# Performance work log

Hardware: AMD Instinct MI355X
Metric: run time of the kernel (lower is better)

Reference implementation:

```python
import jax, jax.numpy as jnp
import numpy as np

N = 50000
E = 1600000
IN_DIM = 32
EDGE_DIM = 32
HID = 64
OUT = 32


def setup_inputs() -> dict:
    key = jax.random.key(0)
    ks = jax.random.split(key, 12)
    x = jax.random.normal(ks[0], (N, IN_DIM), dtype=jnp.float32)
    edge_index = jax.random.randint(ks[1], (2, E), 0, N, dtype=jnp.int64)
    edge_attr = jax.random.normal(ks[2], (E, EDGE_DIM), dtype=jnp.float32)
    # MLP params: Linear(64->64), Linear(64->128), Linear(128->64), Linear(64->32)
    def lin(k, fan_in, fan_out):
        lim = 1.0 / np.sqrt(fan_in)
        kw, kb = jax.random.split(k)
        W = jax.random.uniform(kw, (fan_in, fan_out), minval=-lim, maxval=lim, dtype=jnp.float32)
        b = jax.random.uniform(kb, (fan_out,), minval=-lim, maxval=lim, dtype=jnp.float32)
        return W, b
    W1, b1 = lin(ks[3], IN_DIM + EDGE_DIM, HID)
    W2, b2 = lin(ks[4], HID, 2 * HID)
    W3, b3 = lin(ks[5], 2 * HID, HID)
    W4, b4 = lin(ks[6], HID, OUT)
    return {"x": x, "edge_index": edge_index, "edge_attr": edge_attr,
            "W1": W1, "b1": b1, "W2": W2, "b2": b2,
            "W3": W3, "b3": b3, "W4": W4, "b4": b4}


def reference(x, edge_index, edge_attr, W1, b1, W2, b2, W3, b3, W4, b4):
    # PyG MessagePassing (source_to_target): x_i = x[edge_index[1]] (target),
    # messages aggregated (mean) at target nodes edge_index[1].
    dst = edge_index[1]
    x_i = x[dst]                                   # [E, IN_DIM] gather
    m = jnp.concatenate([x_i, edge_attr], axis=-1)  # [E, 64]
    # 4-layer MLP with ReLU (dropout = identity at inference)
    m = jax.nn.relu(m @ W1 + b1)                   # [E, 64]
    m = jax.nn.relu(m @ W2 + b2)                   # [E, 128]
    m = jax.nn.relu(m @ W3 + b3)                   # [E, 64]
    m = jax.nn.relu(m @ W4 + b4)                   # [E, 32]
    # mean scatter to target nodes
    sums = jax.ops.segment_sum(m, dst, num_segments=N)          # [N, 32]
    cnt = jax.ops.segment_sum(jnp.ones((E,), m.dtype), dst, num_segments=N)
    out = sums / jnp.maximum(cnt, 1.0)[:, None]
    return out
```

## Files before the change

### kernel.cpp

```cpp
#include <hip/hip_runtime.h>
#include <hip/hip_bf16.h>

typedef __attribute__((ext_vector_type(8))) unsigned short u16x8;
typedef __attribute__((ext_vector_type(8))) __bf16 bf16x8;
typedef __attribute__((ext_vector_type(4))) float f32x4;

__device__ __forceinline__ unsigned pack_bf2(float lo, float hi) {
  unsigned a = __float_as_uint(lo) + 0x8000u;
  unsigned b = __float_as_uint(hi) + 0x8000u;
  return __builtin_amdgcn_perm(b, a, 0x07060302);
}

__device__ __forceinline__ unsigned short f2bf(float f) {
  unsigned u = __float_as_uint(f);
  return (unsigned short)((u + 0x7fffu + ((u >> 16) & 1u)) >> 16);
}

__device__ __forceinline__ int aswz(int row, int feat, int stride) {
  return row * stride + (((feat >> 3) ^ (row & 7)) << 4) + (feat & 7) * 2;
}

__global__ __launch_bounds__(256)
void prep_hist(const float* __restrict__ W1, const float* __restrict__ W2,
               const float* __restrict__ W3, const float* __restrict__ W4,
               unsigned short* __restrict__ wt,
               const int* __restrict__ ei, int* __restrict__ histI, int E, int N) {
  const int tid = threadIdx.x;
  const int i = blockIdx.x * 256 + tid;
  if (i < 22528) {
    float v; int n, k, K, base;
    if (i < 4096)       { n = i >> 6, k = i & 63;  K = 64;  base = 0;     v = W1[k * 64 + n]; }
    else if (i < 12288) { int j = i - 4096;  n = j >> 6, k = j & 63;  K = 64;  base = 4096;  v = W2[k * 128 + n]; }
    else if (i < 20480) { int j = i - 12288; n = j >> 7, k = j & 127; K = 128; base = 12288; v = W3[k * 64 + n]; }
    else                { int j = i - 20480; n = j >> 6, k = j & 63;  K = 64;  base = 20480; v = W4[k * 32 + n]; }
    int o = base + n * K + ((((k >> 3) ^ (n & 7)) << 3) + (k & 7));
    wt[o] = f2bf(v);
  }
  const int xcd = blockIdx.x & 7, kblk = blockIdx.x >> 3;
  const int nchunks = gridDim.x >> 3;
  const int chunk = (((E + nchunks - 1) / nchunks) + 3) & ~3;
  const int eBeg = kblk * chunk;
  const int eEnd = min(eBeg + chunk, E);
  const int dLo = (int)((long)xcd * N / 8);
  const int dHi = (int)((long)(xcd + 1) * N / 8);
  int e0 = eBeg + tid * 4;
  for (; e0 + 3 < eEnd; e0 += 1024) {
    const int4 d4 = *(const int4*)(ei + E + e0);
    if (d4.x >= dLo && d4.x < dHi) atomicAdd(&histI[d4.x], 1);
    if (d4.y >= dLo && d4.y < dHi) atomicAdd(&histI[d4.y], 1);
    if (d4.z >= dLo && d4.z < dHi) atomicAdd(&histI[d4.z], 1);
    if (d4.w >= dLo && d4.w < dHi) atomicAdd(&histI[d4.w], 1);
  }
  for (int e = e0; e < eEnd; ++e) {
    const int d = ei[E + e];
    if (d >= dLo && d < dHi) atomicAdd(&histI[d], 1);
  }
}

__global__ void scan_blocks(const int* __restrict__ histI, int* __restrict__ row_start,
                            int* __restrict__ blockSums, int N) {
  __shared__ int wsum[4];
  const int lane = threadIdx.x & 63, w = threadIdx.x >> 6;
  const int i0 = blockIdx.x * 2048 + threadIdx.x * 8;
  int v[8];
#pragma unroll
  for (int j = 0; j < 8; ++j) { int i = i0 + j; v[j] = (i < N) ? histI[i] : 0; }
  int s = 0;
#pragma unroll
  for (int j = 0; j < 8; ++j) { int t = v[j]; v[j] = s; s += t; }
  int ss = s;
#pragma unroll
  for (int d = 1; d < 64; d <<= 1) { int t = __shfl_up(ss, d, 64); if (lane >= d) ss += t; }
  if (lane == 63) wsum[w] = ss;
  __syncthreads();
  int wOff = 0;
#pragma unroll
  for (int k = 0; k < 4; ++k) if (k < w) wOff += wsum[k];
  const int tOff = wOff + (ss - s);
#pragma unroll
  for (int j = 0; j < 8; ++j) { int i = i0 + j; if (i < N) row_start[i] = tOff + v[j]; }
  if (threadIdx.x == 255) blockSums[blockIdx.x] = wOff + ss;
}

__global__ __launch_bounds__(256)
void fill_kernel(const int* __restrict__ ei, int* __restrict__ row_start,
                 const int* __restrict__ blockSums, int2* __restrict__ edlist,
                 float* __restrict__ out, int E, int N, int nb) {
  __shared__ int spre[32];
  if (threadIdx.x == 0) {
    int acc = 0;
    for (int k = 0; k < nb; ++k) { spre[k] = acc; acc += blockSums[k]; }
  }
  __syncthreads();
  const int tid = threadIdx.x;
  const int Ntot4 = N * 8;
  for (int i = blockIdx.x * 256 + tid; i < Ntot4; i += gridDim.x * 256)
    ((float4*)out)[i] = make_float4(0.f, 0.f, 0.f, 0.f);

  const int xcd = blockIdx.x & 7, kblk = blockIdx.x >> 3;
  const int nchunks = gridDim.x >> 3;
  const int chunk = (((E + nchunks - 1) / nchunks) + 3) & ~3;
  const int eBeg = kblk * chunk;
  const int eEnd = min(eBeg + chunk, E);
  const int dLo = (int)((long)xcd * N / 8);
  const int dHi = (int)((long)(xcd + 1) * N / 8);
  int e0 = eBeg + tid * 4;
  for (; e0 + 3 < eEnd; e0 += 1024) {
    const int4 d4 = *(const int4*)(ei + E + e0);
    const int dv[4] = {d4.x, d4.y, d4.z, d4.w};
#pragma unroll
    for (int j = 0; j < 4; ++j) {
      const int d = dv[j];
      if (d >= dLo && d < dHi) {
        const int pos = atomicAdd(&row_start[d], 1) + spre[d >> 11];
        edlist[pos] = make_int2(e0 + j, d);
      }
    }
  }
  for (int e = e0; e < eEnd; ++e) {
    const int d = ei[E + e];
    if (d >= dLo && d < dHi) {
      const int pos = atomicAdd(&row_start[d], 1) + spre[d >> 11];
      edlist[pos] = make_int2(e, d);
    }
  }
}

template <int MT, int KS, int SS, int DS>
__device__ __forceinline__ void mlp_layer(const unsigned char* src, unsigned char* dst,
                                          const unsigned char* wl, const float* biasL, int lane) {
  const int edge = lane & 15, g = lane >> 4;
  asm volatile("s_waitcnt lgkmcnt(0)" ::: "memory");
  u16x8 bfrag[KS];
#pragma unroll
  for (int ks = 0; ks < KS; ++ks)
    bfrag[ks] = *(const u16x8*)(src + aswz(edge, ks * 32 + g * 8, SS));
#pragma unroll
  for (int mt = 0; mt < MT; ++mt) {
    const int n = mt * 16 + edge;
    u16x8 af[KS];
#pragma unroll
    for (int ks = 0; ks < KS; ++ks)
      af[ks] = *(const u16x8*)(wl + n * (KS * 64) + (((ks * 4 + g) ^ (edge & 7)) << 4));
    const float4 bv = *(const float4*)(biasL + mt * 16 + g * 4);
    f32x4 acc = {bv.x, bv.y, bv.z, bv.w};
    __builtin_amdgcn_s_setprio(1);
#pragma unroll
    for (int ks = 0; ks < KS; ++ks)
      acc = __builtin_amdgcn_mfma_f32_16x16x32_bf16(
          __builtin_bit_cast(bf16x8, af[ks]), __builtin_bit_cast(bf16x8, bfrag[ks]),
          acc, 0, 0, 0);
    __builtin_amdgcn_s_setprio(0);
    const int fb = mt * 16 + g * 4;
    uint2 q;
    q.x = pack_bf2(fmaxf(acc[0], 0.f), fmaxf(acc[1], 0.f));
    q.y = pack_bf2(fmaxf(acc[2], 0.f), fmaxf(acc[3], 0.f));
    *(uint2*)(dst + aswz(edge, fb, DS)) = q;
  }
}

__device__ __forceinline__ void load_tile(int ebase, int E, const int2* __restrict__ edlist,
                                          const float* __restrict__ x, const float* __restrict__ ea,
                                          const int* __restrict__ histI,
                                          int lane, float4& xa, float4& xb, float4& ya, float4& yb,
                                          int& dstA, int& cntA) {
  const int el = ebase + (lane >> 2);
  const int part = lane & 3;
  xa = make_float4(0.f, 0.f, 0.f, 0.f); xb = xa; ya = xa; yb = xa;
  if (el < E) {
    const int2 ed = edlist[el];
    const float4* xp = (const float4*)(x + (size_t)ed.y * 32 + part * 8);
    xa = xp[0]; xb = xp[1];
    const float4* ep = (const float4*)(ea + (size_t)ed.x * 32 + part * 8);
    ya = ep[0]; yb = ep[1];
  }
  const int pos = ebase + (lane & 15);
  dstA = -1; cntA = 1;
  if (pos < E) {
    dstA = edlist[pos].y;
    cntA = histI[dstA];
  }
}

#define BIAS_OFF 45056
#define ACT_OFF  46208

__global__ __launch_bounds__(1024, 4)
void gnn_main(const float* __restrict__ x, const int2* __restrict__ edlist,
              const float* __restrict__ ea, const unsigned short* __restrict__ wt,
              const int* __restrict__ histI,
              const float* __restrict__ b1, const float* __restrict__ b2,
              const float* __restrict__ b3, const float* __restrict__ b4,
              float* __restrict__ out, int E, int numTiles) {
  __shared__ __align__(16) unsigned char lds[ACT_OFF + 16 * 6144];
  {
    const u16x8* gw = (const u16x8*)wt;
    u16x8* lw = (u16x8*)lds;
    for (int i = threadIdx.x; i < 2816; i += 1024) lw[i] = gw[i];
    float* biasW = (float*)(lds + BIAS_OFF);
    for (int i = threadIdx.x; i < 288; i += 1024) {
      float v;
      if (i < 64) v = b1[i];
      else if (i < 192) v = b2[i - 64];
      else if (i < 256) v = b3[i - 192];
      else v = b4[i - 256];
      biasW[i] = v;
    }
  }
  __syncthreads();

  const int lane = threadIdx.x & 63, wid = threadIdx.x >> 6;
  const int li = lane & 15, g = lane >> 4;
  const float* biasLds = (const float*)(lds + BIAS_OFF);
  unsigned char* buf0 = lds + ACT_OFF + wid * 6144;
  unsigned char* buf1 = buf0 + 4096;
  const unsigned char* wl1 = lds;
  const unsigned char* wl2 = lds + 8192;
  const unsigned char* wl3 = lds + 24576;
  const unsigned char* wl4 = lds + 40960;

  const int wgl = blockIdx.x * 16 + wid;
  const int wstride = gridDim.x * 16;

  float4 xa, xb, ya, yb; int dstA = -1, cntA = 1;
  if (wgl < numTiles) load_tile(wgl * 16, E, edlist, x, ea, histI, lane, xa, xb, ya, yb, dstA, cntA);

  for (int tile = wgl; tile < numTiles; tile += wstride) {
    uint4 hx, he;
    hx.x = pack_bf2(xa.x, xa.y); hx.y = pack_bf2(xa.z, xa.w);
    hx.z = pack_bf2(xb.x, xb.y); hx.w = pack_bf2(xb.z, xb.w);
    he.x = pack_bf2(ya.x, ya.y); he.y = pack_bf2(ya.z, ya.w);
    he.z = pack_bf2(yb.x, yb.y); he.w = pack_bf2(yb.z, yb.w);
    const int e2 = lane >> 2, part = lane & 3;
    *(uint4*)(buf0 + aswz(e2, part * 8, 256)) = hx;
    *(uint4*)(buf0 + aswz(e2, 32 + part * 8, 256)) = he;

    const int curDst = dstA, curCnt = cntA;

    const int nt = tile + wstride;
    float4 nxa, nxb, nya, nyb; int nd = -1, nc = 1;
    if (nt < numTiles) load_tile(nt * 16, E, edlist, x, ea, histI, lane, nxa, nxb, nya, nyb, nd, nc);
    else { nxa = make_float4(0,0,0,0); nxb = nxa; nya = nxa; nyb = nxa; }

    mlp_layer<4, 2, 256, 128>(buf0, buf1, wl1, biasLds + 0,   lane);
    mlp_layer<8, 2, 128, 256>(buf1, buf0, wl2, biasLds + 64,  lane);
    mlp_layer<4, 4, 256, 128>(buf0, buf1, wl3, biasLds + 192, lane);

    asm volatile("s_waitcnt lgkmcnt(0)" ::: "memory");
    u16x8 bf4[2];
#pragma unroll
    for (int ks = 0; ks < 2; ++ks)
      bf4[ks] = *(const u16x8*)(buf1 + aswz(li, ks * 32 + g * 8, 128));
    float vals[8];
#pragma unroll
    for (int mt = 0; mt < 2; ++mt) {
      const int n = mt * 16 + li;
      u16x8 af[2];
#pragma unroll
      for (int ks = 0; ks < 2; ++ks)
        af[ks] = *(const u16x8*)(wl4 + n * 128 + (((ks * 4 + g) ^ (li & 7)) << 4));
      const float4 bv = *(const float4*)(biasLds + 256 + mt * 16 + g * 4);
      f32x4 acc = {bv.x, bv.y, bv.z, bv.w};
      __builtin_amdgcn_s_setprio(1);
#pragma unroll
      for (int ks = 0; ks < 2; ++ks)
        acc = __builtin_amdgcn_mfma_f32_16x16x32_bf16(
            __builtin_bit_cast(bf16x8, af[ks]), __builtin_bit_cast(bf16x8, bf4[ks]),
            acc, 0, 0, 0);
      __builtin_amdgcn_s_setprio(0);
#pragma unroll
      for (int r = 0; r < 4; ++r) vals[mt * 4 + r] = fmaxf(acc[r], 0.f);
    }

    const int prev = __shfl_up(curDst, 1, 16);
    const bool is_head = (li == 0) || (prev != curDst);
    const unsigned long long hb = __ballot(is_head);
    const unsigned gm = (unsigned)((hb >> (g * 16)) & 0xFFFFu);
    const unsigned below = gm & ((1u << li) | ((1u << li) - 1u));
    const int dist = li - (31 - __clz(below));
#pragma unroll
    for (int d = 1; d < 16; d <<= 1) {
#pragma unroll
      for (int t = 0; t < 8; ++t) {
        const float tv = __shfl_up(vals[t], d, 16);
        if (dist >= d) vals[t] += tv;
      }
    }
    const bool is_end = (li == 15) || ((gm >> (li + 1)) & 1u);
    if (is_end && curDst >= 0) {
      const float inv = 1.0f / (float)curCnt;
      float* op = out + (size_t)curDst * 32 + g * 4;
#pragma unroll
      for (int t = 0; t < 4; ++t) unsafeAtomicAdd(op + t, vals[t] * inv);
#pragma unroll
      for (int t = 0; t < 4; ++t) unsafeAtomicAdd(op + 16 + t, vals[4 + t] * inv);
    }

    xa = nxa; xb = nxb; ya = nya; yb = nyb; dstA = nd; cntA = nc;
  }
}

extern "C" void kernel_launch(void* const* d_in, const int* in_sizes, int n_in,
                              void* d_out, int out_size, void* d_ws, size_t ws_size,
                              hipStream_t stream) {
  const float* x  = (const float*)d_in[0];
  const int*   ei = (const int*)d_in[1];
  const float* ea = (const float*)d_in[2];
  const float* W1 = (const float*)d_in[3];
  const float* b1 = (const float*)d_in[4];
  const float* W2 = (const float*)d_in[5];
  const float* b2 = (const float*)d_in[6];
  const float* W3 = (const float*)d_in[7];
  const float* b3 = (const float*)d_in[8];
  const float* W4 = (const float*)d_in[9];
  const float* b4 = (const float*)d_in[10];
  const int N = in_sizes[0] / 32;
  const int E = in_sizes[1] / 2;
  float* out = (float*)d_out;

  char* ws = (char*)d_ws;
  size_t off = 0;
  auto alloc = [&](size_t bytes) { size_t o = off; off += (bytes + 255) & ~(size_t)255; return o; };
  size_t hist_off = alloc((size_t)N * 4);
  int* histI      = (int*)(ws + hist_off);
  int* row_start  = (int*)(ws + alloc((size_t)(N + 1) * 4));
  int* blockSums  = (int*)(ws + alloc(256 * 4));
  int2* edlist    = (int2*)(ws + alloc((size_t)E * 8));
  unsigned short* wt = (unsigned short*)(ws + alloc(22528 * 2));

  hipMemsetAsync(histI, 0, (size_t)N * 4, stream);

  prep_hist<<<2048, 256, 0, stream>>>(W1, W2, W3, W4, wt, ei, histI, E, N);
  const int nb = (N + 2047) / 2048;
  scan_blocks<<<nb, 256, 0, stream>>>(histI, row_start, blockSums, N);
  fill_kernel<<<2048, 256, 0, stream>>>(ei, row_start, blockSums, edlist, out, E, N, nb);
  const int numTiles = (E + 15) / 16;
  gnn_main<<<256, 1024, 0, stream>>>(x, edlist, ea, wt, histI,
                                     b1, b2, b3, b4, out, E, numTiles);
}
```

Before: 315.7 us.

## Keep MLP activations in registers with 32x32 MFMA and permlane swaps

Replaces the 16x16x32 MFMA layers that staged activations through LDS with 32x32x16 MFMA layers whose outputs are turned into the next layer's B fragments in registers via permlane32_swap. Biases are folded into the pre-swizzled weights as an extra K slice multiplied by a constant-one pad fragment. Tiles grow to 32 edges per wave and the launch shape changes to 768 blocks of 256 threads. The aim is to remove the LDS round trips and waitcnt stalls between layers, at the cost of an extra MFMA per output tile, more registers and a wider segmented scan.

```diff
diff --git a/kernel.cpp b/kernel.cpp
--- a/kernel.cpp
+++ b/kernel.cpp
@@ -3,7 +3,9 @@
 
 typedef __attribute__((ext_vector_type(8))) unsigned short u16x8;
 typedef __attribute__((ext_vector_type(8))) __bf16 bf16x8;
-typedef __attribute__((ext_vector_type(4))) float f32x4;
+typedef __attribute__((ext_vector_type(4))) unsigned uint32x4;
+typedef __attribute__((ext_vector_type(2))) unsigned uint32x2;
+typedef __attribute__((ext_vector_type(16))) float f32x16;
 
 __device__ __forceinline__ unsigned pack_bf2(float lo, float hi) {
   unsigned a = __float_as_uint(lo) + 0x8000u;
@@ -16,24 +18,32 @@
   return (unsigned short)((u + 0x7fffu + ((u >> 16) & 1u)) >> 16);
 }
 
-__device__ __forceinline__ int aswz(int row, int feat, int stride) {
-  return row * stride + (((feat >> 3) ^ (row & 7)) << 4) + (feat & 7) * 2;
-}
-
 __global__ __launch_bounds__(256)
 void prep_hist(const float* __restrict__ W1, const float* __restrict__ W2,
                const float* __restrict__ W3, const float* __restrict__ W4,
+               const float* __restrict__ b1, const float* __restrict__ b2,
+               const float* __restrict__ b3, const float* __restrict__ b4,
                unsigned short* __restrict__ wt,
                const int* __restrict__ ei, int* __restrict__ histI, int E, int N) {
   const int tid = threadIdx.x;
   const int i = blockIdx.x * 256 + tid;
-  if (i < 22528) {
-    float v; int n, k, K, base;
-    if (i < 4096)       { n = i >> 6, k = i & 63;  K = 64;  base = 0;     v = W1[k * 64 + n]; }
-    else if (i < 12288) { int j = i - 4096;  n = j >> 6, k = j & 63;  K = 64;  base = 4096;  v = W2[k * 128 + n]; }
-    else if (i < 20480) { int j = i - 12288; n = j >> 7, k = j & 127; K = 128; base = 12288; v = W3[k * 64 + n]; }
-    else                { int j = i - 20480; n = j >> 6, k = j & 63;  K = 64;  base = 20480; v = W4[k * 32 + n]; }
-    int o = base + n * K + ((((k >> 3) ^ (n & 7)) << 3) + (k & 7));
+  if (i < 22816) {
+    int o; float v;
+    if (i < 22528) {
+      int n, k, S, base;
+      if (i < 4096)       { n = i >> 6;           k = i & 63;  S = 5; base = 0;     v = W1[k * 64 + n]; }
+      else if (i < 12288) { int j = i - 4096;  n = j >> 6;  k = j & 63;  S = 5; base = 5120;  v = W2[k * 128 + n]; }
+      else if (i < 20480) { int j = i - 12288; n = j >> 7;  k = j & 127; S = 9; base = 15360; v = W3[k * 64 + n]; }
+      else                { int j = i - 20480; n = j >> 6;  k = j & 63;  S = 5; base = 24576; v = W4[k * 32 + n]; }
+      const int t = n >> 5, r = n & 31, s = k >> 4, hh = (k >> 3) & 1, jj = k & 7;
+      o = base + ((t * S + s) * 64 + hh * 32 + r) * 8 + jj;
+    } else {
+      const int i2 = i - 22528;
+      if (i2 < 64)       { int q = i2;       int t = q >> 5, r = q & 31; o = 0     + ((t * 5 + 4) * 64 + r) * 8; v = b1[q]; }
+      else if (i2 < 192) { int q = i2 - 64;  int t = q >> 5, r = q & 31; o = 5120  + ((t * 5 + 4) * 64 + r) * 8; v = b2[q]; }
+      else if (i2 < 256) { int q = i2 - 192; int t = q >> 5, r = q & 31; o = 15360 + ((t * 9 + 8) * 64 + r) * 8; v = b3[q]; }
+      else               { int q = i2 - 256; int t = q >> 5, r = q & 31; o = 24576 + ((t * 5 + 4) * 64 + r) * 8; v = b4[q]; }
+    }
     wt[o] = f2bf(v);
   }
   const int xcd = blockIdx.x & 7, kblk = blockIdx.x >> 3;
@@ -126,177 +136,162 @@
   }
 }
 
-template <int MT, int KS, int SS, int DS>
-__device__ __forceinline__ void mlp_layer(const unsigned char* src, unsigned char* dst,
-                                          const unsigned char* wl, const float* biasL, int lane) {
-  const int edge = lane & 15, g = lane >> 4;
-  asm volatile("s_waitcnt lgkmcnt(0)" ::: "memory");
-  u16x8 bfrag[KS];
-#pragma unroll
-  for (int ks = 0; ks < KS; ++ks)
-    bfrag[ks] = *(const u16x8*)(src + aswz(edge, ks * 32 + g * 8, SS));
-#pragma unroll
-  for (int mt = 0; mt < MT; ++mt) {
-    const int n = mt * 16 + edge;
-    u16x8 af[KS];
-#pragma unroll
-    for (int ks = 0; ks < KS; ++ks)
-      af[ks] = *(const u16x8*)(wl + n * (KS * 64) + (((ks * 4 + g) ^ (edge & 7)) << 4));
-    const float4 bv = *(const float4*)(biasL + mt * 16 + g * 4);
-    f32x4 acc = {bv.x, bv.y, bv.z, bv.w};
+__device__ __forceinline__ void c2frag(const f32x16 a, uint32x4& f0, uint32x4& f1) {
+  unsigned u[8];
+#pragma unroll
+  for (int q = 0; q < 4; ++q) {
+    u[2 * q]     = pack_bf2(fmaxf(a[4 * q + 0], 0.f), fmaxf(a[4 * q + 1], 0.f));
+    u[2 * q + 1] = pack_bf2(fmaxf(a[4 * q + 2], 0.f), fmaxf(a[4 * q + 3], 0.f));
+  }
+  const uint32x2 r0 = __builtin_amdgcn_permlane32_swap(u[0], u[2], false, false);
+  const uint32x2 r1 = __builtin_amdgcn_permlane32_swap(u[1], u[3], false, false);
+  const uint32x2 r2 = __builtin_amdgcn_permlane32_swap(u[4], u[6], false, false);
+  const uint32x2 r3 = __builtin_amdgcn_permlane32_swap(u[5], u[7], false, false);
+  f0[0] = r0[0]; f0[1] = r1[0]; f0[2] = r0[1]; f0[3] = r1[1];
+  f1[0] = r2[0]; f1[1] = r3[0]; f1[2] = r2[1]; f1[3] = r3[1];
+}
+
+template <int T, int S>
+__device__ __forceinline__ void layerC(const unsigned char* wl, const uint32x4* bin,
+                                       const uint32x4 padf, uint32x4* bout, int lane) {
+#pragma unroll
+  for (int t = 0; t < T; ++t) {
+    f32x16 a = {};
     __builtin_amdgcn_s_setprio(1);
 #pragma unroll
-    for (int ks = 0; ks < KS; ++ks)
-      acc = __builtin_amdgcn_mfma_f32_16x16x32_bf16(
-          __builtin_bit_cast(bf16x8, af[ks]), __builtin_bit_cast(bf16x8, bfrag[ks]),
-          acc, 0, 0, 0);
+    for (int s = 0; s <= S; ++s) {
+      const u16x8 af = *(const u16x8*)(wl + (size_t)((t * (S + 1) + s) * 64 + lane) * 16);
+      const uint32x4 bb = (s < S) ? bin[s] : padf;
+      a = __builtin_amdgcn_mfma_f32_32x32x16_bf16(
+          __builtin_bit_cast(bf16x8, af), __builtin_bit_cast(bf16x8, bb), a, 0, 0, 0);
+    }
     __builtin_amdgcn_s_setprio(0);
-    const int fb = mt * 16 + g * 4;
-    uint2 q;
-    q.x = pack_bf2(fmaxf(acc[0], 0.f), fmaxf(acc[1], 0.f));
-    q.y = pack_bf2(fmaxf(acc[2], 0.f), fmaxf(acc[3], 0.f));
-    *(uint2*)(dst + aswz(edge, fb, DS)) = q;
-  }
-}
-
-__device__ __forceinline__ void load_tile(int ebase, int E, const int2* __restrict__ edlist,
-                                          const float* __restrict__ x, const float* __restrict__ ea,
-                                          const int* __restrict__ histI,
-                                          int lane, float4& xa, float4& xb, float4& ya, float4& yb,
-                                          int& dstA, int& cntA) {
-  const int el = ebase + (lane >> 2);
-  const int part = lane & 3;
-  xa = make_float4(0.f, 0.f, 0.f, 0.f); xb = xa; ya = xa; yb = xa;
-  if (el < E) {
-    const int2 ed = edlist[el];
-    const float4* xp = (const float4*)(x + (size_t)ed.y * 32 + part * 8);
-    xa = xp[0]; xb = xp[1];
-    const float4* ep = (const float4*)(ea + (size_t)ed.x * 32 + part * 8);
-    ya = ep[0]; yb = ep[1];
-  }
-  const int pos = ebase + (lane & 15);
+    c2frag(a, bout[2 * t], bout[2 * t + 1]);
+  }
+}
+
+__device__ __forceinline__ f32x16 layer4(const unsigned char* wl, const uint32x4* bin,
+                                         const uint32x4 padf, int lane) {
+  f32x16 a = {};
+  __builtin_amdgcn_s_setprio(1);
+#pragma unroll
+  for (int s = 0; s <= 4; ++s) {
+    const u16x8 af = *(const u16x8*)(wl + (size_t)(s * 64 + lane) * 16);
+    const uint32x4 bb = (s < 4) ? bin[s] : padf;
+    a = __builtin_amdgcn_mfma_f32_32x32x16_bf16(
+        __builtin_bit_cast(bf16x8, af), __builtin_bit_cast(bf16x8, bb), a, 0, 0, 0);
+  }
+  __builtin_amdgcn_s_setprio(0);
+  return a;
+}
+
+__device__ __forceinline__ uint32x4 pk8(const float4& a, const float4& b) {
+  uint32x4 r;
+  r[0] = pack_bf2(a.x, a.y); r[1] = pack_bf2(a.z, a.w);
+  r[2] = pack_bf2(b.x, b.y); r[3] = pack_bf2(b.z, b.w);
+  return r;
+}
+
+__device__ __forceinline__ void load_tile32(int pbase, int E, const int2* __restrict__ edlist,
+                                            const float* __restrict__ x, const float* __restrict__ ea,
+                                            const int* __restrict__ histI, int lane,
+                                            float4 (&px)[4], float4 (&pe)[4], int& dstA, int& cntA) {
+  const int pos = pbase + (lane & 31);
+  const int h = lane >> 5;
+#pragma unroll
+  for (int j = 0; j < 4; ++j) { px[j] = make_float4(0.f, 0.f, 0.f, 0.f); pe[j] = px[j]; }
   dstA = -1; cntA = 1;
   if (pos < E) {
-    dstA = edlist[pos].y;
-    cntA = histI[dstA];
-  }
-}
-
-#define BIAS_OFF 45056
-#define ACT_OFF  46208
-
-__global__ __launch_bounds__(1024, 4)
+    const int2 ed = edlist[pos];
+    dstA = ed.y; cntA = histI[ed.y];
+    const float4* xp = (const float4*)(x + (size_t)ed.y * 32);
+    const float4* ep = (const float4*)(ea + (size_t)ed.x * 32);
+    px[0] = xp[2 * h]; px[1] = xp[2 * h + 1]; px[2] = xp[4 + 2 * h]; px[3] = xp[5 + 2 * h];
+    pe[0] = ep[2 * h]; pe[1] = ep[2 * h + 1]; pe[2] = ep[4 + 2 * h]; pe[3] = ep[5 + 2 * h];
+  }
+}
+
+__global__ __launch_bounds__(256, 3)
 void gnn_main(const float* __restrict__ x, const int2* __restrict__ edlist,
               const float* __restrict__ ea, const unsigned short* __restrict__ wt,
-              const int* __restrict__ histI,
-              const float* __restrict__ b1, const float* __restrict__ b2,
-              const float* __restrict__ b3, const float* __restrict__ b4,
-              float* __restrict__ out, int E, int numTiles) {
-  __shared__ __align__(16) unsigned char lds[ACT_OFF + 16 * 6144];
+              const int* __restrict__ histI, float* __restrict__ out, int E, int numTiles) {
+  __shared__ __align__(16) unsigned char lds[54272];
   {
     const u16x8* gw = (const u16x8*)wt;
     u16x8* lw = (u16x8*)lds;
-    for (int i = threadIdx.x; i < 2816; i += 1024) lw[i] = gw[i];
-    float* biasW = (float*)(lds + BIAS_OFF);
-    for (int i = threadIdx.x; i < 288; i += 1024) {
-      float v;
-      if (i < 64) v = b1[i];
-      else if (i < 192) v = b2[i - 64];
-      else if (i < 256) v = b3[i - 192];
-      else v = b4[i - 256];
-      biasW[i] = v;
-    }
+    for (int i = threadIdx.x; i < 3392; i += 256) lw[i] = gw[i];
   }
   __syncthreads();
 
   const int lane = threadIdx.x & 63, wid = threadIdx.x >> 6;
-  const int li = lane & 15, g = lane >> 4;
-  const float* biasLds = (const float*)(lds + BIAS_OFF);
-  unsigned char* buf0 = lds + ACT_OFF + wid * 6144;
-  unsigned char* buf1 = buf0 + 4096;
   const unsigned char* wl1 = lds;
-  const unsigned char* wl2 = lds + 8192;
-  const unsigned char* wl3 = lds + 24576;
-  const unsigned char* wl4 = lds + 40960;
-
-  const int wgl = blockIdx.x * 16 + wid;
-  const int wstride = gridDim.x * 16;
-
-  float4 xa, xb, ya, yb; int dstA = -1, cntA = 1;
-  if (wgl < numTiles) load_tile(wgl * 16, E, edlist, x, ea, histI, lane, xa, xb, ya, yb, dstA, cntA);
+  const unsigned char* wl2 = lds + 10240;
+  const unsigned char* wl3 = lds + 30720;
+  const unsigned char* wl4 = lds + 49152;
+
+  uint32x4 padf;
+  padf[0] = (lane < 32) ? 0x3F80u : 0u;
+  padf[1] = 0u; padf[2] = 0u; padf[3] = 0u;
+
+  const int wgl = blockIdx.x * 4 + wid;
+  const int wstride = gridDim.x * 4;
+
+  float4 px[4], pe[4]; int dstA = -1, cntA = 1;
+  if (wgl < numTiles) load_tile32(wgl * 32, E, edlist, x, ea, histI, lane, px, pe, dstA, cntA);
 
   for (int tile = wgl; tile < numTiles; tile += wstride) {
-    uint4 hx, he;
-    hx.x = pack_bf2(xa.x, xa.y); hx.y = pack_bf2(xa.z, xa.w);
-    hx.z = pack_bf2(xb.x, xb.y); hx.w = pack_bf2(xb.z, xb.w);
-    he.x = pack_bf2(ya.x, ya.y); he.y = pack_bf2(ya.z, ya.w);
-    he.z = pack_bf2(yb.x, yb.y); he.w = pack_bf2(yb.z, yb.w);
-    const int e2 = lane >> 2, part = lane & 3;
-    *(uint4*)(buf0 + aswz(e2, part * 8, 256)) = hx;
-    *(uint4*)(buf0 + aswz(e2, 32 + part * 8, 256)) = he;
-
+    uint32x4 b0[4];
+    b0[0] = pk8(px[0], px[1]);
+    b0[1] = pk8(px[2], px[3]);
+    b0[2] = pk8(pe[0], pe[1]);
+    b0[3] = pk8(pe[2], pe[3]);
     const int curDst = dstA, curCnt = cntA;
 
     const int nt = tile + wstride;
-    float4 nxa, nxb, nya, nyb; int nd = -1, nc = 1;
-    if (nt < numTiles) load_tile(nt * 16, E, edlist, x, ea, histI, lane, nxa, nxb, nya, nyb, nd, nc);
-    else { nxa = make_float4(0,0,0,0); nxb = nxa; nya = nxa; nyb = nxa; }
-
-    mlp_layer<4, 2, 256, 128>(buf0, buf1, wl1, biasLds + 0,   lane);
-    mlp_layer<8, 2, 128, 256>(buf1, buf0, wl2, biasLds + 64,  lane);
-    mlp_layer<4, 4, 256, 128>(buf0, buf1, wl3, biasLds + 192, lane);
-
-    asm volatile("s_waitcnt lgkmcnt(0)" ::: "memory");
-    u16x8 bf4[2];
-#pragma unroll
-    for (int ks = 0; ks < 2; ++ks)
-      bf4[ks] = *(const u16x8*)(buf1 + aswz(li, ks * 32 + g * 8, 128));
-    float vals[8];
-#pragma unroll
-    for (int mt = 0; mt < 2; ++mt) {
-      const int n = mt * 16 + li;
-      u16x8 af[2];
-#pragma unroll
-      for (int ks = 0; ks < 2; ++ks)
-        af[ks] = *(const u16x8*)(wl4 + n * 128 + (((ks * 4 + g) ^ (li & 7)) << 4));
-      const float4 bv = *(const float4*)(biasLds + 256 + mt * 16 + g * 4);
-      f32x4 acc = {bv.x, bv.y, bv.z, bv.w};
-      __builtin_amdgcn_s_setprio(1);
-#pragma unroll
-      for (int ks = 0; ks < 2; ++ks)
-        acc = __builtin_amdgcn_mfma_f32_16x16x32_bf16(
-            __builtin_bit_cast(bf16x8, af[ks]), __builtin_bit_cast(bf16x8, bf4[ks]),
-            acc, 0, 0, 0);
-      __builtin_amdgcn_s_setprio(0);
-#pragma unroll
-      for (int r = 0; r < 4; ++r) vals[mt * 4 + r] = fmaxf(acc[r], 0.f);
-    }
-
-    const int prev = __shfl_up(curDst, 1, 16);
-    const bool is_head = (li == 0) || (prev != curDst);
+    float4 npx[4], npe[4]; int nd = -1, nc = 1;
+    if (nt < numTiles) load_tile32(nt * 32, E, edlist, x, ea, histI, lane, npx, npe, nd, nc);
+    else {
+#pragma unroll
+      for (int j = 0; j < 4; ++j) { npx[j] = make_float4(0.f, 0.f, 0.f, 0.f); npe[j] = npx[j]; }
+    }
+
+    uint32x4 b1[4], b2[8], b3[4];
+    layerC<2, 4>(wl1, b0, padf, b1, lane);
+    layerC<4, 4>(wl2, b1, padf, b2, lane);
+    layerC<2, 8>(wl3, b2, padf, b3, lane);
+    const f32x16 a4 = layer4(wl4, b3, padf, lane);
+
+    float vals[16];
+#pragma unroll
+    for (int r = 0; r < 16; ++r) vals[r] = fmaxf(a4[r], 0.f);
+
+    const int e32 = lane & 31;
+    const int prev = __shfl_up(curDst, 1, 32);
+    const bool is_head = (e32 == 0) || (prev != curDst);
     const unsigned long long hb = __ballot(is_head);
-    const unsigned gm = (unsigned)((hb >> (g * 16)) & 0xFFFFu);
-    const unsigned below = gm & ((1u << li) | ((1u << li) - 1u));
-    const int dist = li - (31 - __clz(below));
-#pragma unroll
-    for (int d = 1; d < 16; d <<= 1) {
-#pragma unroll
-      for (int t = 0; t < 8; ++t) {
-        const float tv = __shfl_up(vals[t], d, 16);
-        if (dist >= d) vals[t] += tv;
+    const unsigned gm = (unsigned)(hb >> ((lane >> 5) << 5));
+    const unsigned below = gm & ((1u << e32) | ((1u << e32) - 1u));
+    const int dist = e32 - (31 - __clz(below));
+#pragma unroll
+    for (int d = 1; d < 32; d <<= 1) {
+#pragma unroll
+      for (int r = 0; r < 16; ++r) {
+        const float tv = __shfl_up(vals[r], d, 32);
+        if (dist >= d) vals[r] += tv;
       }
     }
-    const bool is_end = (li == 15) || ((gm >> (li + 1)) & 1u);
+    const bool is_end = (e32 == 31) || ((gm >> (e32 + 1)) & 1u);
     if (is_end && curDst >= 0) {
       const float inv = 1.0f / (float)curCnt;
-      float* op = out + (size_t)curDst * 32 + g * 4;
-#pragma unroll
-      for (int t = 0; t < 4; ++t) unsafeAtomicAdd(op + t, vals[t] * inv);
-#pragma unroll
-      for (int t = 0; t < 4; ++t) unsafeAtomicAdd(op + 16 + t, vals[4 + t] * inv);
-    }
-
-    xa = nxa; xb = nxb; ya = nya; yb = nyb; dstA = nd; cntA = nc;
+      float* op = out + (size_t)curDst * 32 + 4 * (lane >> 5);
+#pragma unroll
+      for (int r = 0; r < 16; ++r)
+        unsafeAtomicAdd(op + (r & 3) + 8 * (r >> 2), vals[r] * inv);
+    }
+
+#pragma unroll
+    for (int j = 0; j < 4; ++j) { px[j] = npx[j]; pe[j] = npe[j]; }
+    dstA = nd; cntA = nc;
   }
 }
 
@@ -322,19 +317,19 @@
   size_t off = 0;
   auto alloc = [&](size_t bytes) { size_t o = off; off += (bytes + 255) & ~(size_t)255; return o; };
   size_t hist_off = alloc((size_t)N * 4);
+  size_t wt_off   = alloc(27136 * 2);
   int* histI      = (int*)(ws + hist_off);
+  unsigned short* wt = (unsigned short*)(ws + wt_off);
   int* row_start  = (int*)(ws + alloc((size_t)(N + 1) * 4));
   int* blockSums  = (int*)(ws + alloc(256 * 4));
   int2* edlist    = (int2*)(ws + alloc((size_t)E * 8));
-  unsigned short* wt = (unsigned short*)(ws + alloc(22528 * 2));
-
-  hipMemsetAsync(histI, 0, (size_t)N * 4, stream);
-
-  prep_hist<<<2048, 256, 0, stream>>>(W1, W2, W3, W4, wt, ei, histI, E, N);
+
+  hipMemsetAsync(ws + hist_off, 0, (wt_off - hist_off) + 27136 * 2, stream);
+
+  prep_hist<<<2048, 256, 0, stream>>>(W1, W2, W3, W4, b1, b2, b3, b4, wt, ei, histI, E, N);
   const int nb = (N + 2047) / 2048;
   scan_blocks<<<nb, 256, 0, stream>>>(histI, row_start, blockSums, N);
   fill_kernel<<<2048, 256, 0, stream>>>(ei, row_start, blockSums, edlist, out, E, N, nb);
-  const int numTiles = (E + 15) / 16;
-  gnn_main<<<256, 1024, 0, stream>>>(x, edlist, ea, wt, histI,
-                                     b1, b2, b3, b4, out, E, numTiles);
-}
+  const int numTiles = (E + 31) / 32;
+  gnn_main<<<768, 256, 0, stream>>>(x, edlist, ea, wt, histI, out, E, numTiles);
+}
```

Result: slower. 744.1 us (+135.7%).
